# Optimization experiments

Hardware: AMD Instinct MI355X
Metric: run time of the kernel (lower is better)

Reference implementation:

```python
import jax, jax.numpy as jnp
import numpy as np

B, S, V, D, F, NC = 256, 64, 100000, 64, 10, 10  # batch, seq, vocab, emb_dim, n_feats, n_clusters


def setup_inputs() -> dict:
    key = jax.random.key(0)
    ks = jax.random.split(key, 12)
    ids = jax.random.randint(ks[0], (B, S), 0, V)
    emb_table = jax.random.normal(ks[1], (V, D), dtype=jnp.float32) * 0.02
    comb_w1 = jax.random.normal(ks[2], (2 * D, D), dtype=jnp.float32) / np.sqrt(2 * D)
    comb_b1 = jnp.zeros((D,), jnp.float32)
    comb_w2 = jax.random.normal(ks[3], (D, F), dtype=jnp.float32) / np.sqrt(D)
    comb_b2 = jnp.zeros((F,), jnp.float32)
    freq_w1 = jax.random.normal(ks[4], (D + 1, D), dtype=jnp.float32) / np.sqrt(D + 1)
    freq_b1 = jnp.zeros((D,), jnp.float32)
    freq_w2 = jax.random.normal(ks[5], (D, F), dtype=jnp.float32) / np.sqrt(D)
    freq_b2 = jnp.zeros((F,), jnp.float32)
    cluster_centers = jax.random.normal(ks[6], (NC, D), dtype=jnp.float32)
    cat_freq = jnp.ones((V,), jnp.float32)          # category_frequencies buffer
    total_samples = jnp.array(1.0, jnp.float32)     # total_samples buffer
    return dict(category_ids=ids, emb_table=emb_table,
                comb_w1=comb_w1, comb_b1=comb_b1, comb_w2=comb_w2, comb_b2=comb_b2,
                freq_w1=freq_w1, freq_b1=freq_b1, freq_w2=freq_w2, freq_b2=freq_b2,
                cluster_centers=cluster_centers, cat_freq=cat_freq,
                total_samples=total_samples)


def reference(category_ids, emb_table, comb_w1, comb_b1, comb_w2, comb_b2,
              freq_w1, freq_b1, freq_w2, freq_b2, cluster_centers,
              cat_freq, total_samples):
    emb = emb_table[category_ids]                      # [B,S,D]
    # --- pairwise combination features (vectorized over all i<j pairs) ---
    iu, ju = np.triu_indices(S, 1)                     # P = S*(S-1)/2 pairs
    P = iu.shape[0]
    pairs = jnp.concatenate([emb[:, iu], emb[:, ju]], axis=-1)   # [B,P,2D]
    h = jax.nn.relu(jnp.einsum('bpe,ed->bpd', pairs, comb_w1) + comb_b1)
    combo = jnp.einsum('bpd,df->bpf', h, comb_w2) + comb_b2      # [B,P,F]
    combo_sum = combo.sum(axis=1)                      # [B,F]
    # --- frequency features ---
    freqs = cat_freq[category_ids] / total_samples     # [B,S]
    freq_in = jnp.concatenate([emb, freqs[..., None]], axis=-1)  # [B,S,D+1]
    fh = jax.nn.relu(jnp.einsum('bse,ed->bsd', freq_in, freq_w1) + freq_b1)
    freq_feat = jnp.einsum('bsd,df->bsf', fh, freq_w2) + freq_b2  # [B,S,F]
    # --- cluster assignment features (softmax over -euclidean distances) ---
    d2 = (jnp.sum(emb * emb, axis=-1, keepdims=True)
          + jnp.sum(cluster_centers * cluster_centers, axis=-1)
          - 2.0 * jnp.einsum('bsd,cd->bsc', emb, cluster_centers))
    dist = jnp.sqrt(jnp.maximum(d2, 0.0))              # [B,S,NC]
    cluster_feat = jax.nn.softmax(-dist, axis=-1)      # [B,S,F] (F==NC)
    # --- mean over stacked features: freq + P pair feats (broadcast over seq) + cluster ---
    out = (freq_feat + combo_sum[:, None, :] + cluster_feat) / (P + 2)
    return out
```

## Files before the change

### kernel.cpp

```cpp
#include <hip/hip_runtime.h>
#include <math.h>


typedef _Float16 h2 __attribute__((ext_vector_type(2)));
typedef _Float16 h4 __attribute__((ext_vector_type(4)));

constexpr int BATCH = 256;
constexpr int S = 64, D = 64, F = 10;
constexpr int NPAIR = S * (S - 1) / 2;

constexpr int EMBS = 6144;
constexpr int U2B  = 8192;
constexpr int V2B  = 10240;
constexpr int FHT  = 12288;
constexpr int EMBT = 12288;
constexpr int CF_F = 14400;
constexpr int DI_F = 15040;
constexpr int W2P  = 15680;
constexpr int PART_F = 0;
constexpr int FF_F   = 2048;
constexpr int HS_F   = 2688;
constexpr int CS_F   = 2752;

__device__ __forceinline__ h2 pk2(float a, float b) {
#if __has_builtin(__builtin_amdgcn_cvt_pkrtz)
  auto t = __builtin_amdgcn_cvt_pkrtz(a, b);
  return __builtin_bit_cast(h2, t);
#else
  h2 r; r.x = (_Float16)a; r.y = (_Float16)b; return r;
#endif
}

__device__ __forceinline__ float fdot2f(h2 a, h2 b, float c) {
#if __has_builtin(__builtin_amdgcn_fdot2)
  typedef __fp16 q2 __attribute__((ext_vector_type(2)));
  return __builtin_amdgcn_fdot2(__builtin_bit_cast(q2, a),
                                __builtin_bit_cast(q2, b), c, false);
#else
  return c + (float)a.x * (float)b.x + (float)a.y * (float)b.y;
#endif
}

__device__ __forceinline__ h2 hmax2z(h2 a) {
#if __has_builtin(__builtin_elementwise_max)
  h2 z = {(_Float16)0, (_Float16)0};
  return __builtin_elementwise_max(a, z);
#else
  h2 r;
  r.x = a.x > (_Float16)0 ? a.x : (_Float16)0;
  r.y = a.y > (_Float16)0 ? a.y : (_Float16)0;
  return r;
#endif
}

__device__ __forceinline__ float lane_up1(float v) {
#if __has_builtin(__builtin_amdgcn_update_dpp)
  int r = __builtin_amdgcn_update_dpp(0, __float_as_int(v), 0xF5, 0xF, 0xF, false);
  return __int_as_float(r);
#else
  return __shfl_down(v, 1, 64);
#endif
}

__global__ __launch_bounds__(1024, 4)
void cat_enc_kernel(const int*   __restrict__ ids,
                    const float* __restrict__ emb_table,
                    const float* __restrict__ comb_w1,
                    const float* __restrict__ comb_b1,
                    const float* __restrict__ comb_w2,
                    const float* __restrict__ comb_b2,
                    const float* __restrict__ freq_w1,
                    const float* __restrict__ freq_b1,
                    const float* __restrict__ freq_w2,
                    const float* __restrict__ freq_b2,
                    const float* __restrict__ centers,
                    const float* __restrict__ cat_freq,
                    const float* __restrict__ total_samples,
                    float*       __restrict__ out)
{
  __shared__ __align__(16) unsigned int ldsu[16000];
  h2*    ldsH = (h2*)ldsu;
  float* ldsf = (float*)ldsu;
  const int tid = threadIdx.x;
  const int b = blockIdx.x, bBase = b * S;

  {
    for (int task = tid; task < 3072; task += 1024) {
      int mat = task >> 10, r = task & 1023, k4 = r >> 6, d = r & 63;
      const float* src = (mat == 0) ? (comb_w1 + (k4 * 4) * D + d)
                       : (mat == 1) ? (comb_w1 + (D + k4 * 4) * D + d)
                                    : (freq_w1 + (k4 * 4) * D + d);
      float w0 = src[0], w1 = src[D], w2v = src[2 * D], w3 = src[3 * D];
      ldsH[mat * 2048 + k4 * 64 + d]        = pk2(w0, w1);
      ldsH[mat * 2048 + 1024 + k4 * 64 + d] = pk2(w2v, w3);
    }
    int s = tid >> 4, q = tid & 15;
    int id = ids[bBase + s];
    float4 e4 = *(const float4*)(emb_table + (size_t)id * D + q * 4);
    h2 p0 = pk2(e4.x, e4.y), p1 = pk2(e4.z, e4.w);
    ldsH[EMBS + s * 32 + q * 2]     = p0;
    ldsH[EMBS + s * 32 + q * 2 + 1] = p1;
    ldsH[EMBT + (q * 2) * 64 + s]     = p0;
    ldsH[EMBT + (q * 2 + 1) * 64 + s] = p1;
    if (tid < 320) {
      int d2 = tid / 10, f = tid - d2 * 10;
      ldsH[W2P + tid] = pk2(freq_w2[(2 * d2) * F + f], freq_w2[(2 * d2 + 1) * F + f]);
    }
  }
  __syncthreads();

  {
    int wv = __builtin_amdgcn_readfirstlane((int)(tid >> 6));
    int lane = tid & 63;
    if (wv < 10) {
      const float* crow = centers + wv * D;
      float acc = 0.f;
#pragma unroll 8
      for (int k2 = 0; k2 < 32; ++k2) {
        h2 e2 = ldsH[EMBT + k2 * 64 + lane];
        float t0 = (float)e2.x - crow[2 * k2];
        float t1 = (float)e2.y - crow[2 * k2 + 1];
        acc = fmaf(t0, t0, fmaf(t1, t1, acc));
      }
      ldsf[DI_F + lane * 10 + wv] = sqrtf(acc);
    }
  }
  __syncthreads();

  {
    const int d  = tid & 63;
    const int wv = __builtin_amdgcn_readfirstlane((int)(tid >> 6));
    const int s0 = wv * 4;
    const float invT = 1.0f / total_samples[0];
    int idv[4];
#pragma unroll
    for (int si = 0; si < 4; ++si)
      idv[si] = __builtin_amdgcn_readfirstlane(ids[bBase + s0 + si]);
    const float b1d = comb_b1[d], fb1d = freq_b1[d], fw1L = freq_w1[D * D + d];
    float aU[4], aV[4], aF[4];
#pragma unroll
    for (int si = 0; si < 4; ++si) {
      aU[si] = b1d; aV[si] = 0.f;
      aF[si] = fmaf(cat_freq[idv[si]] * invT, fw1L, fb1d);
    }
#pragma unroll 4
    for (int k4 = 0; k4 < 16; ++k4) {
      h2 wul = ldsH[k4 * 64 + d],        wuh = ldsH[1024 + k4 * 64 + d];
      h2 wvl = ldsH[2048 + k4 * 64 + d], wvh = ldsH[3072 + k4 * 64 + d];
      h2 wfl = ldsH[4096 + k4 * 64 + d], wfh = ldsH[5120 + k4 * 64 + d];
#pragma unroll
      for (int si = 0; si < 4; ++si) {
        h4 e = *(const h4*)&ldsH[EMBS + (s0 + si) * 32 + k4 * 2];
        h2 el = e.lo, eh = e.hi;
        aU[si] = fdot2f(el, wul, aU[si]); aU[si] = fdot2f(eh, wuh, aU[si]);
        aV[si] = fdot2f(el, wvl, aV[si]); aV[si] = fdot2f(eh, wvh, aV[si]);
        aF[si] = fdot2f(el, wfl, aF[si]); aF[si] = fdot2f(eh, wfh, aF[si]);
      }
    }
    const bool evenl = ((d & 1) == 0);
    const int d2 = d >> 1;
#pragma unroll
    for (int si = 0; si < 4; ++si) {
      float un = lane_up1(aU[si]);
      float vn = lane_up1(aV[si]);
      float fh = fmaxf(aF[si], 0.f);
      float fn = lane_up1(fh);
      if (evenl) {
        int srow = s0 + si;
        ldsH[U2B + srow * 32 + d2] = pk2(aU[si], un);
        ldsH[V2B + srow * 32 + d2] = pk2(aV[si], vn);
        ldsH[FHT + srow * 33 + d2] = pk2(fh, fn);
      }
    }
  }
  __syncthreads();

  {
    if (tid < 640) {
      int s = tid & 63;
      int f = __builtin_amdgcn_readfirstlane((int)(tid >> 6));
      float acc = freq_b2[f];
#pragma unroll 8
      for (int d2 = 0; d2 < 32; ++d2)
        acc = fdot2f(ldsH[FHT + s * 33 + d2], ldsH[W2P + d2 * 10 + f], acc);
      ldsf[FF_F + s * 10 + f] = acc;
    } else if (tid < 704) {
      int s = tid - 640;
      float dv[10], dmin = 1e30f;
#pragma unroll
      for (int c = 0; c < 10; ++c) { dv[c] = ldsf[DI_F + s * 10 + c]; dmin = fminf(dmin, dv[c]); }
      float p[10], sum = 0.f;
#pragma unroll
      for (int c = 0; c < 10; ++c) { p[c] = expf(dmin - dv[c]); sum += p[c]; }
      float rs = 1.0f / sum;
#pragma unroll
      for (int c = 0; c < 10; ++c) ldsf[CF_F + s * 10 + c] = p[c] * rs;
    }
  }

  {
    const int dg = tid & 31, g = tid >> 5;
    h2 u2a = ldsH[U2B + g * 32 + dg];
    h2 u2b = ldsH[U2B + (63 - g) * 32 + dg];
    h2 za = {(_Float16)0, (_Float16)0};
    h2 acca = za, accb = za;
    const int jsplit = 64 - g;
#pragma unroll 4
    for (int j = g + 1; j < 64; ++j) {
      h2 v2 = ldsH[V2B + j * 32 + dg];
      acca = acca + hmax2z(u2a + v2);
      if (j >= jsplit) accb = accb + hmax2z(u2b + v2);
    }
    h2 at = acca + accb;
    ldsf[PART_F + g * 64 + 2 * dg]     = (float)at.x;
    ldsf[PART_F + g * 64 + 2 * dg + 1] = (float)at.y;
  }
  __syncthreads();

  if (tid < 64) {
    float h = 0.f;
#pragma unroll
    for (int g = 0; g < 32; ++g) h += ldsf[PART_F + g * 64 + tid];
    ldsf[HS_F + tid] = h;
  }
  __syncthreads();

  if (tid < 10) {
    float cs = comb_b2[tid] * (float)NPAIR;
#pragma unroll 8
    for (int dd = 0; dd < 64; ++dd)
      cs = fmaf(ldsf[HS_F + dd], comb_w2[dd * F + tid], cs);
    ldsf[CS_F + tid] = cs;
  }
  __syncthreads();

  if (tid < 640) {
    int f = tid % 10;
    float val = (ldsf[FF_F + tid] + ldsf[CS_F + f] + ldsf[CF_F + tid])
              * (1.0f / (float)(NPAIR + 2));
    out[(size_t)b * 640 + tid] = val;
  }
}

extern "C" void kernel_launch(void* const* d_in, const int* in_sizes, int n_in,
                              void* d_out, int out_size, void* d_ws, size_t ws_size,
                              hipStream_t stream) {
  (void)in_sizes; (void)n_in; (void)d_ws; (void)ws_size; (void)out_size;
  const int*   ids        = (const int*)  d_in[0];
  const float* emb_table  = (const float*)d_in[1];
  const float* comb_w1    = (const float*)d_in[2];
  const float* comb_b1    = (const float*)d_in[3];
  const float* comb_w2    = (const float*)d_in[4];
  const float* comb_b2    = (const float*)d_in[5];
  const float* freq_w1    = (const float*)d_in[6];
  const float* freq_b1    = (const float*)d_in[7];
  const float* freq_w2    = (const float*)d_in[8];
  const float* freq_b2    = (const float*)d_in[9];
  const float* centers    = (const float*)d_in[10];
  const float* cat_freq   = (const float*)d_in[11];
  const float* total_samp = (const float*)d_in[12];
  float* out = (float*)d_out;

  hipLaunchKernelGGL(cat_enc_kernel, dim3(BATCH), dim3(1024), 0, stream,
                     ids, emb_table, comb_w1, comb_b1, comb_w2, comb_b2,
                     freq_w1, freq_b1, freq_w2, freq_b2, centers, cat_freq,
                     total_samp, out);
}
```

Baseline: 110.7 us.

## Widen LDS vector loads, transpose V layout, and fuse the final reduction stages

Repacks the W1 weights into LDS as interleaved h4/h8 blocks so the projection loop reads 8 halves per load. It also transposes the V matrix (with a padded stride) so the pairwise ReLU loop loads two j values per h4 read, and widens the freq_w2 dot product the same way. The separate h-sum and comb_w2 stages are merged into one wave-level shuffle reduction, which removes one __syncthreads. This reduces LDS instruction count and barrier overhead, at the cost of more complex indexing and possible bank conflicts from the new strides.

```diff
diff --git a/kernel.cpp b/kernel.cpp
--- a/kernel.cpp
+++ b/kernel.cpp
@@ -4,6 +4,9 @@
 
 typedef _Float16 h2 __attribute__((ext_vector_type(2)));
 typedef _Float16 h4 __attribute__((ext_vector_type(4)));
+typedef _Float16 h8 __attribute__((ext_vector_type(8)));
+union H4u { h4 v; h2 h[2]; };
+union H8u { h8 v; h2 h[4]; };
 
 constexpr int BATCH = 256;
 constexpr int S = 64, D = 64, F = 10;
@@ -11,15 +14,14 @@
 
 constexpr int EMBS = 6144;
 constexpr int U2B  = 8192;
-constexpr int V2B  = 10240;
-constexpr int FHT  = 12288;
-constexpr int EMBT = 12288;
-constexpr int CF_F = 14400;
-constexpr int DI_F = 15040;
-constexpr int W2P  = 15680;
+constexpr int V2T  = 10240;
+constexpr int FHT  = 12352;
+constexpr int EMBT = 12352;
+constexpr int CF_F = 14528;
+constexpr int DI_F = 15168;
+constexpr int W2P  = 15808;
 constexpr int PART_F = 0;
 constexpr int FF_F   = 2048;
-constexpr int HS_F   = 2688;
 constexpr int CS_F   = 2752;
 
 __device__ __forceinline__ h2 pk2(float a, float b) {
@@ -78,22 +80,13 @@
                     const float* __restrict__ total_samples,
                     float*       __restrict__ out)
 {
-  __shared__ __align__(16) unsigned int ldsu[16000];
+  __shared__ __align__(16) unsigned int ldsu[16128];
   h2*    ldsH = (h2*)ldsu;
   float* ldsf = (float*)ldsu;
   const int tid = threadIdx.x;
   const int b = blockIdx.x, bBase = b * S;
 
   {
-    for (int task = tid; task < 3072; task += 1024) {
-      int mat = task >> 10, r = task & 1023, k4 = r >> 6, d = r & 63;
-      const float* src = (mat == 0) ? (comb_w1 + (k4 * 4) * D + d)
-                       : (mat == 1) ? (comb_w1 + (D + k4 * 4) * D + d)
-                                    : (freq_w1 + (k4 * 4) * D + d);
-      float w0 = src[0], w1 = src[D], w2v = src[2 * D], w3 = src[3 * D];
-      ldsH[mat * 2048 + k4 * 64 + d]        = pk2(w0, w1);
-      ldsH[mat * 2048 + 1024 + k4 * 64 + d] = pk2(w2v, w3);
-    }
     int s = tid >> 4, q = tid & 15;
     int id = ids[bBase + s];
     float4 e4 = *(const float4*)(emb_table + (size_t)id * D + q * 4);
@@ -102,8 +95,22 @@
     ldsH[EMBS + s * 32 + q * 2 + 1] = p1;
     ldsH[EMBT + (q * 2) * 64 + s]     = p0;
     ldsH[EMBT + (q * 2 + 1) * 64 + s] = p1;
+
+    {
+      const int k4 = tid >> 6, dd = tid & 63;
+      const float* s0p = comb_w1 + (k4 * 4) * D + dd;
+      const float* s1p = s0p + D * D;
+      const float* s2p = freq_w1 + (k4 * 4) * D + dd;
+      h4* dst = (h4*)ldsu;
+      H4u u0; u0.h[0] = pk2(s0p[0], s0p[D]); u0.h[1] = pk2(s0p[2 * D], s0p[3 * D]);
+      H4u u1; u1.h[0] = pk2(s1p[0], s1p[D]); u1.h[1] = pk2(s1p[2 * D], s1p[3 * D]);
+      H4u u2; u2.h[0] = pk2(s2p[0], s2p[D]); u2.h[1] = pk2(s2p[2 * D], s2p[3 * D]);
+      dst[2 * tid]     = u0.v;
+      dst[2 * tid + 1] = u1.v;
+      dst[2048 + tid]  = u2.v;
+    }
     if (tid < 320) {
-      int d2 = tid / 10, f = tid - d2 * 10;
+      int f = tid >> 5, d2 = tid & 31;
       ldsH[W2P + tid] = pk2(freq_w2[(2 * d2) * F + f], freq_w2[(2 * d2 + 1) * F + f]);
     }
   }
@@ -143,18 +150,30 @@
       aU[si] = b1d; aV[si] = 0.f;
       aF[si] = fmaf(cat_freq[idv[si]] * invT, fw1L, fb1d);
     }
-#pragma unroll 4
-    for (int k4 = 0; k4 < 16; ++k4) {
-      h2 wul = ldsH[k4 * 64 + d],        wuh = ldsH[1024 + k4 * 64 + d];
-      h2 wvl = ldsH[2048 + k4 * 64 + d], wvh = ldsH[3072 + k4 * 64 + d];
-      h2 wfl = ldsH[4096 + k4 * 64 + d], wfh = ldsH[5120 + k4 * 64 + d];
+    const h8* WUVp = (const h8*)ldsu;
+    const h4* WFp  = (const h4*)(ldsu + 4096);
+#pragma unroll 2
+    for (int k8 = 0; k8 < 8; ++k8) {
+      const int k4a = 2 * k8, k4b = 2 * k8 + 1;
+      H8u wa; wa.v = WUVp[k4a * 64 + d];
+      H8u wb; wb.v = WUVp[k4b * 64 + d];
+      H4u fa; fa.v = WFp[k4a * 64 + d];
+      H4u fb; fb.v = WFp[k4b * 64 + d];
 #pragma unroll
       for (int si = 0; si < 4; ++si) {
-        h4 e = *(const h4*)&ldsH[EMBS + (s0 + si) * 32 + k4 * 2];
-        h2 el = e.lo, eh = e.hi;
-        aU[si] = fdot2f(el, wul, aU[si]); aU[si] = fdot2f(eh, wuh, aU[si]);
-        aV[si] = fdot2f(el, wvl, aV[si]); aV[si] = fdot2f(eh, wvh, aV[si]);
-        aF[si] = fdot2f(el, wfl, aF[si]); aF[si] = fdot2f(eh, wfh, aF[si]);
+        H8u e; e.v = *(const h8*)&ldsH[EMBS + (s0 + si) * 32 + k8 * 4];
+        aU[si] = fdot2f(e.h[0], wa.h[0], aU[si]);
+        aU[si] = fdot2f(e.h[1], wa.h[1], aU[si]);
+        aV[si] = fdot2f(e.h[0], wa.h[2], aV[si]);
+        aV[si] = fdot2f(e.h[1], wa.h[3], aV[si]);
+        aF[si] = fdot2f(e.h[0], fa.h[0], aF[si]);
+        aF[si] = fdot2f(e.h[1], fa.h[1], aF[si]);
+        aU[si] = fdot2f(e.h[2], wb.h[0], aU[si]);
+        aU[si] = fdot2f(e.h[3], wb.h[1], aU[si]);
+        aV[si] = fdot2f(e.h[2], wb.h[2], aV[si]);
+        aV[si] = fdot2f(e.h[3], wb.h[3], aV[si]);
+        aF[si] = fdot2f(e.h[2], fb.h[0], aF[si]);
+        aF[si] = fdot2f(e.h[3], fb.h[1], aF[si]);
       }
     }
     const bool evenl = ((d & 1) == 0);
@@ -168,8 +187,8 @@
       if (evenl) {
         int srow = s0 + si;
         ldsH[U2B + srow * 32 + d2] = pk2(aU[si], un);
-        ldsH[V2B + srow * 32 + d2] = pk2(aV[si], vn);
-        ldsH[FHT + srow * 33 + d2] = pk2(fh, fn);
+        ldsH[V2T + d2 * 66 + srow] = pk2(aV[si], vn);
+        ldsH[FHT + srow * 34 + d2] = pk2(fh, fn);
       }
     }
   }
@@ -180,9 +199,17 @@
       int s = tid & 63;
       int f = __builtin_amdgcn_readfirstlane((int)(tid >> 6));
       float acc = freq_b2[f];
-#pragma unroll 8
-      for (int d2 = 0; d2 < 32; ++d2)
-        acc = fdot2f(ldsH[FHT + s * 33 + d2], ldsH[W2P + d2 * 10 + f], acc);
+      const h8* wrow = (const h8*)&ldsH[W2P + f * 32];
+#pragma unroll
+      for (int d8 = 0; d8 < 4; ++d8) {
+        H8u wf; wf.v = wrow[d8];
+        H4u f0; f0.v = *(const h4*)&ldsH[FHT + s * 34 + d8 * 4];
+        H4u f1; f1.v = *(const h4*)&ldsH[FHT + s * 34 + d8 * 4 + 2];
+        acc = fdot2f(f0.h[0], wf.h[0], acc);
+        acc = fdot2f(f0.h[1], wf.h[1], acc);
+        acc = fdot2f(f1.h[0], wf.h[2], acc);
+        acc = fdot2f(f1.h[1], wf.h[3], acc);
+      }
       ldsf[FF_F + s * 10 + f] = acc;
     } else if (tid < 704) {
       int s = tid - 640;
@@ -203,15 +230,25 @@
     h2 u2a = ldsH[U2B + g * 32 + dg];
     h2 u2b = ldsH[U2B + (63 - g) * 32 + dg];
     h2 za = {(_Float16)0, (_Float16)0};
-    h2 acca = za, accb = za;
+    h2 acA0 = za, acA1 = za, accb = za;
     const int jsplit = 64 - g;
+    int j = g + 1;
+    if (j & 1) {
+      h2 v2 = ldsH[V2T + dg * 66 + j];
+      acA0 = acA0 + hmax2z(u2a + v2);
+      ++j;
+    }
 #pragma unroll 4
-    for (int j = g + 1; j < 64; ++j) {
-      h2 v2 = ldsH[V2B + j * 32 + dg];
-      acca = acca + hmax2z(u2a + v2);
-      if (j >= jsplit) accb = accb + hmax2z(u2b + v2);
-    }
-    h2 at = acca + accb;
+    for (; j < 64; j += 2) {
+      H4u v; v.v = *(const h4*)&ldsH[V2T + dg * 66 + j];
+      acA0 = acA0 + hmax2z(u2a + v.h[0]);
+      acA1 = acA1 + hmax2z(u2a + v.h[1]);
+      if (j + 1 >= jsplit) {
+        if (j >= jsplit) accb = accb + hmax2z(u2b + v.h[0]);
+        accb = accb + hmax2z(u2b + v.h[1]);
+      }
+    }
+    h2 at = acA0 + acA1 + accb;
     ldsf[PART_F + g * 64 + 2 * dg]     = (float)at.x;
     ldsf[PART_F + g * 64 + 2 * dg + 1] = (float)at.y;
   }
@@ -220,17 +257,16 @@
   if (tid < 64) {
     float h = 0.f;
 #pragma unroll
-    for (int g = 0; g < 32; ++g) h += ldsf[PART_F + g * 64 + tid];
-    ldsf[HS_F + tid] = h;
-  }
-  __syncthreads();
-
-  if (tid < 10) {
-    float cs = comb_b2[tid] * (float)NPAIR;
-#pragma unroll 8
-    for (int dd = 0; dd < 64; ++dd)
-      cs = fmaf(ldsf[HS_F + dd], comb_w2[dd * F + tid], cs);
-    ldsf[CS_F + tid] = cs;
+    for (int g2 = 0; g2 < 32; ++g2) h += ldsf[PART_F + g2 * 64 + tid];
+    float csv = 0.f;
+#pragma unroll
+    for (int f = 0; f < 10; ++f) {
+      float p = h * comb_w2[tid * F + f];
+#pragma unroll
+      for (int off = 1; off < 64; off <<= 1) p += __shfl_xor(p, off, 64);
+      if (tid == f) csv = p;
+    }
+    if (tid < 10) ldsf[CS_F + tid] = fmaf(comb_b2[tid], (float)NPAIR, csv);
   }
   __syncthreads();
 
```

Result: faster. 105.1 us (-5.0%).
